# Kernel optimization log

Hardware: AMD Instinct MI355X
Metric: run time of the kernel (lower is better)

The kernel has to match this reference:

```python
import jax, jax.numpy as jnp
import numpy as np


def _iir_forward(b_coeff, rho, psi, u_in, y_init, u_init):
    # Coefficient computation: stable 2nd-order resonator parameterization
    r = jax.nn.sigmoid(rho)
    theta = jnp.pi * jax.nn.sigmoid(psi)
    a1 = -2.0 * r * jnp.cos(theta)
    a2 = r * r

    B, T = u_in.shape
    nb = b_coeff.shape[0]  # number of FIR taps (n_b)

    # FIR (moving-average) part, fully vectorized over batch and time:
    # v[t] = sum_k b[k] * u[t-k]; past inputs come from u_init = [u[-1], u[-2], ...]
    u_ext = jnp.concatenate([u_init[:, ::-1], u_in], axis=1)  # [B, T + nb - 1], time-ordered
    v = jnp.zeros_like(u_in)
    for k in range(nb):  # small fixed loop over filter taps
        v = v + b_coeff[k] * jax.lax.dynamic_slice_in_dim(u_ext, nb - 1 - k, T, axis=1)

    # AR (recursive) part: y[t] = v[t] - a1*y[t-1] - a2*y[t-2]  (sequential scan over time)
    def step(carry, v_t):
        y1, y2 = carry  # y[t-1], y[t-2], each [B]
        y = v_t - a1 * y1 - a2 * y2
        return (y, y1), y

    init = (y_init[:, 0], y_init[:, 1])  # [y[-1], y[-2]] per lfiltic convention
    _, y = jax.lax.scan(step, init, v.T)  # y: [T, B]
    return y.T  # [B, T]


def setup_inputs() -> dict:
    key = jax.random.key(0)
    k1, k2, k3, k4 = jax.random.split(key, 4)
    B, T, NB = 1024, 16384, 3
    return {
        "b_coeff": 0.1 * jax.random.normal(k1, (NB,), dtype=jnp.float32),
        "rho": jnp.asarray(jax.random.normal(k2, (), dtype=jnp.float32) + 0.9),
        "psi": jnp.asarray(jax.random.normal(k3, (), dtype=jnp.float32) * 0.5),
        "u_in": jax.random.normal(k4, (B, T), dtype=jnp.float32),
        "y_init": jnp.zeros((B, 2), dtype=jnp.float32),
        "u_init": jnp.zeros((B, NB - 1), dtype=jnp.float32),
    }


def reference(b_coeff, rho, psi, u_in, y_init, u_init):
    return _iir_forward(b_coeff, rho, psi, u_in, y_init, u_init)
```

## Files before the change

### kernel.cpp

```cpp
#include <hip/hip_runtime.h>
#include <math.h>


#define TLEN     16384
#define HALF     8192
#define NT       256
#define CK       32
#define NCH      256
#define SCAN_OFF   8450
#define CARRY_OFF  (SCAN_OFF + 2*NCH)
#define LDS_FLOATS (CARRY_OFF + 2)

__device__ __forceinline__ void mat2_sq(float& m00, float& m01, float& m10, float& m11) {
    float t00 = m00*m00 + m01*m10;
    float t01 = m00*m01 + m01*m11;
    float t10 = m10*m00 + m11*m10;
    float t11 = m10*m01 + m11*m11;
    m00 = t00; m01 = t01; m10 = t10; m11 = t11;
}

__global__ __launch_bounds__(NT, 4)
void iir_kernel(const float* __restrict__ bc,
                const float* __restrict__ rho_p,
                const float* __restrict__ psi_p,
                const float* __restrict__ u_in,
                const float* __restrict__ y_init,
                const float* __restrict__ u_init,
                float* __restrict__ y_out)
{
    __shared__ float lds[LDS_FLOATS];
    const int row = blockIdx.x;
    const int tid = threadIdx.x;

    const float rho = rho_p[0];
    const float psi = psi_p[0];
    const float r   = 1.0f / (1.0f + expf(-rho));
    const float th  = 3.14159265358979323846f / (1.0f + expf(-psi));
    const float a1  = -2.0f * r * cosf(th);
    const float a2  = r * r;
    const float b0  = bc[0], b1 = bc[1], b2 = bc[2];

    const float* urow = u_in  + (size_t)row * TLEN;
    float*       orow = y_out + (size_t)row * TLEN;

    for (int h = 0; h < 2; ++h) {
        const float* uh = urow + h * HALF;

        #pragma unroll
        for (int k = 0; k < 8; ++k) {
            int g = tid + k * NT;
            float4 uv = ((const float4*)uh)[g];
            int base = 4*g + 3 + (g >> 3);
            lds[base + 0] = uv.x;
            lds[base + 1] = uv.y;
            lds[base + 2] = uv.z;
            lds[base + 3] = uv.w;
        }
        if (tid == 0) {
            lds[0] = (h == 0) ? u_init[2*row + 1] : urow[h*HALF - 2];
            lds[1] = (h == 0) ? u_init[2*row + 0] : urow[h*HALF - 1];
        }
        __syncthreads();

        const int ub = 33 * tid;
        float um2 = lds[ub];
        float um1 = lds[ub + 1];
        float v[CK];
        float y1 = 0.0f, y2 = 0.0f;
        #pragma unroll
        for (int j = 0; j < CK; ++j) {
            float uc = lds[ub + 3 + j];
            float vv = fmaf(b2, um2, fmaf(b1, um1, b0 * uc));
            v[j] = vv;
            float y = fmaf(-a1, y1, fmaf(-a2, y2, vv));
            y2 = y1; y1 = y;
            um2 = um1; um1 = uc;
        }
        lds[SCAN_OFF + 2*tid]     = y1;
        lds[SCAN_OFF + 2*tid + 1] = y2;
        __syncthreads();

        if (tid < 64) {
            const int l = tid;
            float m00 = -a1, m01 = -a2, m10 = 1.0f, m11 = 0.0f;
            #pragma unroll
            for (int s = 0; s < 5; ++s) mat2_sq(m00, m01, m10, m11);

            float da[4], db[4];
            #pragma unroll
            for (int m = 0; m < 4; ++m) {
                da[m] = lds[SCAN_OFF + 8*l + 2*m];
                db[m] = lds[SCAN_OFF + 8*l + 2*m + 1];
            }

            float seed0 = 0.0f, seed1 = 0.0f;
            if (l == 0) {
                if (h == 0) { seed0 = y_init[2*row]; seed1 = y_init[2*row + 1]; }
                else        { seed0 = lds[CARRY_OFF]; seed1 = lds[CARRY_OFF + 1]; }
            }
            float s0 = seed0, s1 = seed1;
            #pragma unroll
            for (int m = 0; m < 4; ++m) {
                float n0 = fmaf(m00, s0, fmaf(m01, s1, da[m]));
                float n1 = fmaf(m10, s0, fmaf(m11, s1, db[m]));
                s0 = n0; s1 = n1;
            }
            float w00 = m00, w01 = m01, w10 = m10, w11 = m11;
            mat2_sq(w00, w01, w10, w11);
            mat2_sq(w00, w01, w10, w11);
            #pragma unroll
            for (int p = 0; p < 6; ++p) {
                float o0 = __shfl_up(s0, 1 << p);
                float o1 = __shfl_up(s1, 1 << p);
                if (l >= (1 << p)) {
                    s0 = fmaf(w00, o0, fmaf(w01, o1, s0));
                    s1 = fmaf(w10, o0, fmaf(w11, o1, s1));
                }
                if (p < 5) mat2_sq(w00, w01, w10, w11);
            }
            float p0 = __shfl_up(s0, 1);
            float p1 = __shfl_up(s1, 1);
            if (l == 0) { p0 = seed0; p1 = seed1; }
            float c0 = p0, c1 = p1;
            #pragma unroll
            for (int m = 0; m < 4; ++m) {
                lds[SCAN_OFF + 2*(4*l + m)]     = c0;
                lds[SCAN_OFF + 2*(4*l + m) + 1] = c1;
                float n0 = fmaf(m00, c0, fmaf(m01, c1, da[m]));
                float n1 = fmaf(m10, c0, fmaf(m11, c1, db[m]));
                c0 = n0; c1 = n1;
            }
        }
        __syncthreads();

        float y1f = lds[SCAN_OFF + 2*tid];
        float y2f = lds[SCAN_OFF + 2*tid + 1];
        #pragma unroll
        for (int j = 0; j < CK; ++j) {
            float y = fmaf(-a1, y1f, fmaf(-a2, y2f, v[j]));
            lds[ub + 3 + j] = y;
            y2f = y1f; y1f = y;
        }
        if (tid == NT - 1) {
            lds[CARRY_OFF]     = y1f;
            lds[CARRY_OFF + 1] = y2f;
        }
        __syncthreads();

        float* oh = orow + h * HALF;
        #pragma unroll
        for (int k = 0; k < 8; ++k) {
            int g = tid + k * NT;
            int base = 4*g + 3 + (g >> 3);
            float4 ov;
            ov.x = lds[base + 0];
            ov.y = lds[base + 1];
            ov.z = lds[base + 2];
            ov.w = lds[base + 3];
            ((float4*)oh)[g] = ov;
        }
        __syncthreads();
    }
}

extern "C" void kernel_launch(void* const* d_in, const int* in_sizes, int n_in,
                              void* d_out, int out_size, void* d_ws, size_t ws_size,
                              hipStream_t stream) {
    const float* bc    = (const float*)d_in[0];
    const float* rho   = (const float*)d_in[1];
    const float* psi   = (const float*)d_in[2];
    const float* u_in  = (const float*)d_in[3];
    const float* y_in  = (const float*)d_in[4];
    const float* u_ini = (const float*)d_in[5];
    float* y = (float*)d_out;
    const int B = in_sizes[3] / TLEN;
    iir_kernel<<<B, NT, 0, stream>>>(bc, rho, psi, u_in, y_in, u_ini, y);
}
```

Measured before the change: 124.3 us.

## Load inputs directly to registers and drop LDS staging; prefetch second half

Each thread now reads its own 32 contiguous inputs from global memory into registers and writes its outputs straight to global, so the large padded LDS transpose buffer and its barriers go away, leaving only a small scan buffer. The second half's inputs are prefetched during the first half's scan, and the barriers become lightweight lgkmcnt waits plus s_barrier. The cost is uncoalesced per-thread strided float4 accesses (128-byte stride across lanes), more register pressure from holding 32 inputs, and a reliance on hand-placed waitcnt for correctness of the global load/LDS ordering.

```diff
diff --git a/kernel.cpp b/kernel.cpp
--- a/kernel.cpp
+++ b/kernel.cpp
@@ -2,14 +2,13 @@
 #include <math.h>
 
 
-#define TLEN     16384
-#define HALF     8192
-#define NT       256
-#define CK       32
-#define NCH      256
-#define SCAN_OFF   8450
-#define CARRY_OFF  (SCAN_OFF + 2*NCH)
-#define LDS_FLOATS (CARRY_OFF + 2)
+#define TLEN  16384
+#define HALF  8192
+#define NT    256
+#define CK    32
+#define NCH   256
+#define CARRY_OFF (2*NCH)
+#define LDS_FLOATS (2*NCH + 2)
 
 __device__ __forceinline__ void mat2_sq(float& m00, float& m01, float& m10, float& m11) {
     float t00 = m00*m00 + m01*m10;
@@ -17,6 +16,12 @@
     float t10 = m10*m00 + m11*m10;
     float t11 = m10*m01 + m11*m11;
     m00 = t00; m01 = t01; m10 = t10; m11 = t11;
+}
+
+__device__ __forceinline__ void bar_lgkm() {
+    asm volatile("s_waitcnt lgkmcnt(0)" ::: "memory");
+    __builtin_amdgcn_s_barrier();
+    __builtin_amdgcn_sched_barrier(0);
 }
 
 __global__ __launch_bounds__(NT, 4)
@@ -32,6 +37,24 @@
     const int row = blockIdx.x;
     const int tid = threadIdx.x;
 
+    const float* urow = u_in  + (size_t)row * TLEN;
+    float*       orow = y_out + (size_t)row * TLEN;
+
+    float4 uv[8];
+    {
+        const float4* up = (const float4*)(urow + CK * tid);
+        #pragma unroll
+        for (int j = 0; j < 8; ++j) uv[j] = up[j];
+    }
+    float hm2, hm1;
+    if (tid == 0) {
+        hm2 = u_init[2*row + 1];
+        hm1 = u_init[2*row + 0];
+    } else {
+        float2 hh = *(const float2*)(urow + CK*tid - 2);
+        hm2 = hh.x; hm1 = hh.y;
+    }
+
     const float rho = rho_p[0];
     const float psi = psi_p[0];
     const float r   = 1.0f / (1.0f + expf(-rho));
@@ -40,45 +63,40 @@
     const float a2  = r * r;
     const float b0  = bc[0], b1 = bc[1], b2 = bc[2];
 
-    const float* urow = u_in  + (size_t)row * TLEN;
-    float*       orow = y_out + (size_t)row * TLEN;
+    float v[CK];
 
+    #pragma unroll
     for (int h = 0; h < 2; ++h) {
-        const float* uh = urow + h * HALF;
+        float um2 = hm2, um1 = hm1;
+        float y1 = 0.0f, y2 = 0.0f;
+        #define STEP(UC, IDX) {                                        \
+            float uc_ = (UC);                                          \
+            float vv_ = fmaf(b2, um2, fmaf(b1, um1, b0 * uc_));        \
+            v[IDX] = vv_;                                              \
+            float y_ = fmaf(-a1, y1, fmaf(-a2, y2, vv_));              \
+            y2 = y1; y1 = y_;                                          \
+            um2 = um1; um1 = uc_; }
+        #pragma unroll
+        for (int q = 0; q < 8; ++q) {
+            float4 u4 = uv[q];
+            STEP(u4.x, 4*q + 0);
+            STEP(u4.y, 4*q + 1);
+            STEP(u4.z, 4*q + 2);
+            STEP(u4.w, 4*q + 3);
+        }
+        #undef STEP
 
-        #pragma unroll
-        for (int k = 0; k < 8; ++k) {
-            int g = tid + k * NT;
-            float4 uv = ((const float4*)uh)[g];
-            int base = 4*g + 3 + (g >> 3);
-            lds[base + 0] = uv.x;
-            lds[base + 1] = uv.y;
-            lds[base + 2] = uv.z;
-            lds[base + 3] = uv.w;
+        *(float2*)&lds[2*tid] = make_float2(y1, y2);
+
+        if (h == 0) {
+            const float4* up = (const float4*)(urow + HALF + CK * tid);
+            #pragma unroll
+            for (int j = 0; j < 8; ++j) uv[j] = up[j];
+            float2 hh = *(const float2*)(urow + HALF + CK*tid - 2);
+            hm2 = hh.x; hm1 = hh.y;
         }
-        if (tid == 0) {
-            lds[0] = (h == 0) ? u_init[2*row + 1] : urow[h*HALF - 2];
-            lds[1] = (h == 0) ? u_init[2*row + 0] : urow[h*HALF - 1];
-        }
-        __syncthreads();
 
-        const int ub = 33 * tid;
-        float um2 = lds[ub];
-        float um1 = lds[ub + 1];
-        float v[CK];
-        float y1 = 0.0f, y2 = 0.0f;
-        #pragma unroll
-        for (int j = 0; j < CK; ++j) {
-            float uc = lds[ub + 3 + j];
-            float vv = fmaf(b2, um2, fmaf(b1, um1, b0 * uc));
-            v[j] = vv;
-            float y = fmaf(-a1, y1, fmaf(-a2, y2, vv));
-            y2 = y1; y1 = y;
-            um2 = um1; um1 = uc;
-        }
-        lds[SCAN_OFF + 2*tid]     = y1;
-        lds[SCAN_OFF + 2*tid + 1] = y2;
-        __syncthreads();
+        bar_lgkm();
 
         if (tid < 64) {
             const int l = tid;
@@ -86,12 +104,10 @@
             #pragma unroll
             for (int s = 0; s < 5; ++s) mat2_sq(m00, m01, m10, m11);
 
-            float da[4], db[4];
-            #pragma unroll
-            for (int m = 0; m < 4; ++m) {
-                da[m] = lds[SCAN_OFF + 8*l + 2*m];
-                db[m] = lds[SCAN_OFF + 8*l + 2*m + 1];
-            }
+            float4 q0 = *(const float4*)&lds[8*l];
+            float4 q1 = *(const float4*)&lds[8*l + 4];
+            float da[4] = {q0.x, q0.z, q1.x, q1.z};
+            float db[4] = {q0.y, q0.w, q1.y, q1.w};
 
             float seed0 = 0.0f, seed1 = 0.0f;
             if (l == 0) {
@@ -124,42 +140,32 @@
             float c0 = p0, c1 = p1;
             #pragma unroll
             for (int m = 0; m < 4; ++m) {
-                lds[SCAN_OFF + 2*(4*l + m)]     = c0;
-                lds[SCAN_OFF + 2*(4*l + m) + 1] = c1;
+                *(float2*)&lds[2*(4*l + m)] = make_float2(c0, c1);
                 float n0 = fmaf(m00, c0, fmaf(m01, c1, da[m]));
                 float n1 = fmaf(m10, c0, fmaf(m11, c1, db[m]));
                 c0 = n0; c1 = n1;
             }
+            if (l == 63 && h == 0) {
+                lds[CARRY_OFF]     = c0;
+                lds[CARRY_OFF + 1] = c1;
+            }
         }
-        __syncthreads();
+        bar_lgkm();
 
-        float y1f = lds[SCAN_OFF + 2*tid];
-        float y2f = lds[SCAN_OFF + 2*tid + 1];
+        float2 inc = *(const float2*)&lds[2*tid];
+        float y1f = inc.x, y2f = inc.y;
+        float* oh = orow + h * HALF + CK * tid;
         #pragma unroll
-        for (int j = 0; j < CK; ++j) {
-            float y = fmaf(-a1, y1f, fmaf(-a2, y2f, v[j]));
-            lds[ub + 3 + j] = y;
-            y2f = y1f; y1f = y;
+        for (int q = 0; q < 8; ++q) {
+            float ya = fmaf(-a1, y1f, fmaf(-a2, y2f, v[4*q + 0]));
+            float yb = fmaf(-a1, ya,  fmaf(-a2, y1f, v[4*q + 1]));
+            float yc = fmaf(-a1, yb,  fmaf(-a2, ya,  v[4*q + 2]));
+            float yd = fmaf(-a1, yc,  fmaf(-a2, yb,  v[4*q + 3]));
+            float4 w; w.x = ya; w.y = yb; w.z = yc; w.w = yd;
+            *(float4*)(oh + 4*q) = w;
+            y2f = yc; y1f = yd;
         }
-        if (tid == NT - 1) {
-            lds[CARRY_OFF]     = y1f;
-            lds[CARRY_OFF + 1] = y2f;
-        }
-        __syncthreads();
-
-        float* oh = orow + h * HALF;
-        #pragma unroll
-        for (int k = 0; k < 8; ++k) {
-            int g = tid + k * NT;
-            int base = 4*g + 3 + (g >> 3);
-            float4 ov;
-            ov.x = lds[base + 0];
-            ov.y = lds[base + 1];
-            ov.z = lds[base + 2];
-            ov.w = lds[base + 3];
-            ((float4*)oh)[g] = ov;
-        }
-        __syncthreads();
+        if (h == 0) bar_lgkm();
     }
 }
 
```

New measurement: 132.1 us. +6.3%, slower.
